# Kernel tuning notes

Hardware: AMD Instinct MI355X
Metric: run time of the kernel (lower is better)

The kernel has to match this reference:

```python
import jax, jax.numpy as jnp
import numpy as np

EMB_DIM = 1024
NUM_HEADS = 16
HEAD_DIM = EMB_DIM // NUM_HEADS


def setup_inputs() -> dict:
    key = jax.random.key(0)
    ks = jax.random.split(key, 10)
    B, Sq, Skv = 4, 4096, 4096
    scale = 1.0 / np.sqrt(EMB_DIM)
    inp = {
        "query": jax.random.normal(ks[0], (B, Sq, EMB_DIM), jnp.float32),
        "key_value": jax.random.normal(ks[1], (B, Skv, EMB_DIM), jnp.float32),
        "Wq": jax.random.normal(ks[2], (EMB_DIM, EMB_DIM), jnp.float32) * scale,
        "bq": jnp.zeros((EMB_DIM,), jnp.float32),
        "Wk": jax.random.normal(ks[3], (EMB_DIM, EMB_DIM), jnp.float32) * scale,
        "bk": jnp.zeros((EMB_DIM,), jnp.float32),
        "Wv": jax.random.normal(ks[4], (EMB_DIM, EMB_DIM), jnp.float32) * scale,
        "bv": jnp.zeros((EMB_DIM,), jnp.float32),
        "Wo": jax.random.normal(ks[5], (EMB_DIM, EMB_DIM), jnp.float32) * scale,
        "bo": jnp.zeros((EMB_DIM,), jnp.float32),
    }
    return inp


def reference(query, key_value, Wq, bq, Wk, bk, Wv, bv, Wo, bo):
    B, Sq, D = query.shape
    Skv = key_value.shape[1]
    H, hd = NUM_HEADS, HEAD_DIM
    # Projections -> [B, S, H, hd]
    Q = (query @ Wq + bq).reshape(B, Sq, H, hd)
    K = (key_value @ Wk + bk).reshape(B, Skv, H, hd)
    V = (key_value @ Wv + bv).reshape(B, Skv, H, hd)
    # elu+1 feature map (strictly positive)
    Q = jax.nn.elu(Q) + 1.0
    K = jax.nn.elu(K) + 1.0
    # KV summarization: [B, H, hd, hd]
    KV = jnp.einsum("bshd,bshe->bhde", K, V)
    K_sum = K.sum(axis=1)  # [B, H, hd]
    # Attention output and normalizer
    out = jnp.einsum("bqhd,bhde->bqhe", Q, KV)          # [B, Sq, H, hd]
    norm = jnp.einsum("bqhd,bhd->bqh", Q, K_sum)         # [B, Sq, H]
    out = out / (norm[..., None] + 1e-6)
    out = out.reshape(B, Sq, D)
    return out @ Wo + bo  # dropout is identity in eval
```

## Files before the change

kernel.cpp:

```cpp
#include <hip/hip_runtime.h>

typedef __bf16 bf16_t;
typedef __bf16 bf16x2 __attribute__((ext_vector_type(2)));
typedef __bf16 bf16x8 __attribute__((ext_vector_type(8)));
typedef float floatx4 __attribute__((ext_vector_type(4)));

#define B_ 4
#define S_ 4096
#define D_ 1024
#define H_ 16
#define HD_ 64
#define M_TOT (B_ * S_)

__device__ __forceinline__ void async_load16(const bf16_t* g, bf16_t* l) {
  __builtin_amdgcn_global_load_lds(
      (const __attribute__((address_space(1))) void*)g,
      (__attribute__((address_space(3))) void*)l,
      16, 0, 0);
}

struct PrepArgs {
  const float* q; const float* kv;
  bf16_t* aq; bf16_t* akv;
  const float* w0; const float* w1; const float* w2; const float* w3;
  bf16_t* t0; bf16_t* t1; bf16_t* t2; bf16_t* t3;
};

__global__ __launch_bounds__(256) void prep_kernel(PrepArgs p) {
  __shared__ float tile[32][33];
  const int bid = blockIdx.x;
  const int t = threadIdx.x;
  if (bid < 16384) {
    const float* in = bid < 8192 ? p.q : p.kv;
    bf16_t* out = bid < 8192 ? p.aq : p.akv;
    int i = ((bid & 8191) * 256 + t) * 8;
    float4 a = *(const float4*)(in + i);
    float4 b = *(const float4*)(in + i + 4);
    bf16x8 o;
    o[0] = (bf16_t)a.x; o[1] = (bf16_t)a.y; o[2] = (bf16_t)a.z; o[3] = (bf16_t)a.w;
    o[4] = (bf16_t)b.x; o[5] = (bf16_t)b.y; o[6] = (bf16_t)b.z; o[7] = (bf16_t)b.w;
    *(bf16x8*)(out + i) = o;
  } else {
    int idx = bid - 16384;
    int z = idx >> 10;
    int rem = idx & 1023;
    const float* W = z == 0 ? p.w0 : z == 1 ? p.w1 : z == 2 ? p.w2 : p.w3;
    bf16_t* Wt = z == 0 ? p.t0 : z == 1 ? p.t1 : z == 2 ? p.t2 : p.t3;
    int n0 = (rem & 31) * 32;
    int k0 = (rem >> 5) * 32;
    int tx = t & 31;
    int ty = t >> 5;
    for (int r = ty; r < 32; r += 8)
      tile[r][tx] = W[(size_t)(k0 + r) * D_ + n0 + tx];
    __syncthreads();
    for (int r = ty; r < 32; r += 8)
      Wt[(size_t)(n0 + r) * D_ + k0 + tx] = (bf16_t)tile[tx][r];
  }
}

__device__ __forceinline__ void gemm256_core(
    const bf16_t* __restrict__ A, const bf16_t* __restrict__ Bt,
    int row0, int col0, bf16_t* As, bf16_t* Bs, floatx4 (&acc)[8][4]) {
  const int tid = threadIdx.x;
  const int w = tid >> 6;
  const int lane = tid & 63;
  const int lr = lane & 15;
  const int lq = lane >> 4;
  const int wm0 = (w >> 2) * 128;
  const int wn0 = (w & 3) * 64;

  const int c0 = w * 64 + lane;
  const int c1 = c0 + 512;
  const int r0 = c0 >> 2, q0 = c0 & 3;
  const int r1 = c1 >> 2, q1 = c1 & 3;
  const size_t offA0 = (size_t)(row0 + r0) * D_ + ((q0 ^ ((r0 >> 1) & 3)) * 8);
  const size_t offA1 = (size_t)(row0 + r1) * D_ + ((q1 ^ ((r1 >> 1) & 3)) * 8);
  const size_t offB0 = (size_t)(col0 + r0) * D_ + ((q0 ^ ((r0 >> 1) & 3)) * 8);
  const size_t offB1 = (size_t)(col0 + r1) * D_ + ((q1 ^ ((r1 >> 1) & 3)) * 8);
  const int ldst0 = w * 512;
  const int ldst1 = 4096 + w * 512;
  const int swz = (lq ^ ((lr >> 1) & 3)) * 8;

#define STAGE_TILE(tt)                                   \
  {                                                      \
    bf16_t* as_ = As + ((tt) & 3) * 8192;                \
    bf16_t* bs_ = Bs + ((tt) & 3) * 8192;                \
    const int ko_ = (tt) * 32;                           \
    async_load16(A + offA0 + ko_, as_ + ldst0);          \
    async_load16(A + offA1 + ko_, as_ + ldst1);          \
    async_load16(Bt + offB0 + ko_, bs_ + ldst0);         \
    async_load16(Bt + offB1 + ko_, bs_ + ldst1);         \
  }

  STAGE_TILE(0)
  STAGE_TILE(1)

  for (int kt = 0; kt < 32; ++kt) {
    if (kt < 30) {
      STAGE_TILE(kt + 2)
      asm volatile("s_waitcnt vmcnt(8)\n\ts_barrier" ::: "memory");
    } else if (kt == 30) {
      asm volatile("s_waitcnt vmcnt(4)\n\ts_barrier" ::: "memory");
    } else {
      asm volatile("s_waitcnt vmcnt(0)\n\ts_barrier" ::: "memory");
    }
    const bf16_t* as = As + (kt & 3) * 8192;
    const bf16_t* bs = Bs + (kt & 3) * 8192;
    bf16x8 af[8], bfr[4];
#pragma unroll
    for (int i = 0; i < 8; ++i)
      af[i] = *(const bf16x8*)&as[(wm0 + i * 16 + lr) * 32 + swz];
#pragma unroll
    for (int j = 0; j < 4; ++j)
      bfr[j] = *(const bf16x8*)&bs[(wn0 + j * 16 + lr) * 32 + swz];
    __builtin_amdgcn_s_setprio(1);
#pragma unroll
    for (int i = 0; i < 8; ++i)
#pragma unroll
      for (int j = 0; j < 4; ++j)
        acc[i][j] = __builtin_amdgcn_mfma_f32_16x16x32_bf16(af[i], bfr[j], acc[i][j], 0, 0, 0);
    __builtin_amdgcn_s_setprio(0);
  }
#undef STAGE_TILE
}

struct ProjArgs {
  const bf16_t* Aq; const bf16_t* Akv;
  const bf16_t* WqT; const bf16_t* WkvT;
  const float* bq; const float* bk; const float* bv;
  bf16_t* Qf; bf16_t* Kf; bf16_t* Vf;
};

__global__ __launch_bounds__(512, 2) void proj256_kernel(ProjArgs p) {
  __shared__ __attribute__((aligned(16))) bf16_t As[4 * 8192];
  __shared__ __attribute__((aligned(16))) bf16_t Bs[4 * 8192];
  const unsigned L = blockIdx.x;
  const unsigned xcd = L & 7;
  const unsigned slot = L >> 3;
  const unsigned mq = slot / 24u;
  const unsigned s24 = slot % 24u;
  const int mt = xcd * 8 + mq * 2 + (s24 & 1);
  const int nt = s24 >> 1;
  const bool isQ = nt < 4;
  const int row0 = mt * 256;
  const int col0 = (isQ ? nt : nt - 4) * 256;
  const bf16_t* A = isQ ? p.Aq : p.Akv;
  const bf16_t* Bt = isQ ? p.WqT : p.WkvT;

  floatx4 acc[8][4];
#pragma unroll
  for (int i = 0; i < 8; ++i)
#pragma unroll
    for (int j = 0; j < 4; ++j) acc[i][j] = (floatx4){0.f, 0.f, 0.f, 0.f};

  gemm256_core(A, Bt, row0, col0, As, Bs, acc);

  const int tid = threadIdx.x;
  const int w = tid >> 6;
  const int lane = tid & 63;
  const int lr = lane & 15;
  const int lq = lane >> 4;
  const int wm0 = (w >> 2) * 128;
  const int wn0 = (w & 3) * 64;

  if (isQ) {
#pragma unroll
    for (int i = 0; i < 8; ++i) {
      int gr = row0 + wm0 + i * 16 + lq * 4;
#pragma unroll
      for (int j = 0; j < 4; ++j) {
        int gc = col0 + wn0 + j * 16 + lr;
        float bsv = p.bq[gc];
#pragma unroll
        for (int r = 0; r < 4; ++r) {
          float v = acc[i][j][r] + bsv;
          v = v > 0.f ? v + 1.f : __expf(v);
          p.Qf[(size_t)(gr + r) * D_ + gc] = (bf16_t)v;
        }
      }
    }
  } else if (nt < 8) {
#pragma unroll
    for (int i = 0; i < 8; ++i) {
      int gr = row0 + wm0 + i * 16 + lq * 4;
#pragma unroll
      for (int j = 0; j < 4; ++j) {
        int gc = col0 + wn0 + j * 16 + lr;
        float bsv = p.bk[gc];
#pragma unroll
        for (int r = 0; r < 4; ++r) {
          float v = acc[i][j][r] + bsv;
          v = v > 0.f ? v + 1.f : __expf(v);
          p.Kf[(size_t)(gr + r) * D_ + gc] = (bf16_t)v;
        }
      }
    }
  } else {
#pragma unroll
    for (int i = 0; i < 8; ++i) {
      int gr = row0 + wm0 + i * 16 + lq * 4;
#pragma unroll
      for (int j = 0; j < 4; ++j) {
        int gc = col0 + wn0 + j * 16 + lr;
        int vc = gc - 1024;
        float bsv = p.bv[vc];
#pragma unroll
        for (int r = 0; r < 4; ++r) {
          float v = acc[i][j][r] + bsv;
          p.Vf[(size_t)(gr + r) * D_ + vc] = (bf16_t)v;
        }
      }
    }
  }
}

__global__ __launch_bounds__(512, 2) void gemm_out256_kernel(
    const bf16_t* __restrict__ A,
    const bf16_t* __restrict__ Bt,
    const float* __restrict__ bias,
    float* __restrict__ outf) {
  __shared__ __attribute__((aligned(16))) bf16_t As[4 * 8192];
  __shared__ __attribute__((aligned(16))) bf16_t Bs[4 * 8192];
  const unsigned L = blockIdx.x;
  const unsigned xcd = L & 7;
  const unsigned slot = L >> 3;
  const unsigned mq = slot >> 3;
  const unsigned s8 = slot & 7;
  const int mt = xcd * 8 + mq * 2 + (s8 & 1);
  const int nt = s8 >> 1;
  const int row0 = mt * 256;
  const int col0 = nt * 256;

  floatx4 acc[8][4];
#pragma unroll
  for (int i = 0; i < 8; ++i)
#pragma unroll
    for (int j = 0; j < 4; ++j) acc[i][j] = (floatx4){0.f, 0.f, 0.f, 0.f};

  gemm256_core(A, Bt, row0, col0, As, Bs, acc);

  const int tid = threadIdx.x;
  const int w = tid >> 6;
  const int lane = tid & 63;
  const int lr = lane & 15;
  const int lq = lane >> 4;
  const int wm0 = (w >> 2) * 128;
  const int wn0 = (w & 3) * 64;

#pragma unroll
  for (int i = 0; i < 8; ++i) {
    int gr = row0 + wm0 + i * 16 + lq * 4;
#pragma unroll
    for (int j = 0; j < 4; ++j) {
      int gc = col0 + wn0 + j * 16 + lr;
      float bsv = bias[gc];
#pragma unroll
      for (int r = 0; r < 4; ++r)
        outf[(size_t)(gr + r) * D_ + gc] = acc[i][j][r] + bsv;
    }
  }
}

#define KVP 68
__global__ __launch_bounds__(256) void kv_mfma_kernel(
    const bf16_t* __restrict__ Kf, const bf16_t* __restrict__ Vf,
    float* __restrict__ KVpart, float* __restrict__ Kspart) {
  __shared__ __attribute__((aligned(16))) bf16_t Kt[64 * KVP];
  __shared__ __attribute__((aligned(16))) bf16_t Vt[64 * KVP];
  const int t = threadIdx.x;
  const int w = t >> 6, lane = t & 63;
  const int lr = lane & 15, lq = lane >> 4;
  const int bh = blockIdx.x, sc = blockIdx.y;
  const int b = bh >> 4, h = bh & 15;
  const size_t base = (size_t)b * S_ * D_ + (size_t)h * HD_;
  const int p = t >> 3;
  const int c0 = (t & 7) * 8;

  floatx4 acc[4], accn[4];
#pragma unroll
  for (int j = 0; j < 4; ++j) {
    acc[j] = (floatx4){0.f, 0.f, 0.f, 0.f};
    accn[j] = (floatx4){0.f, 0.f, 0.f, 0.f};
  }
  bf16x8 ones;
#pragma unroll
  for (int u = 0; u < 8; ++u) ones[u] = (bf16_t)(lr == 0 ? 1.f : 0.f);

  for (int st = 0; st < 8; ++st) {
    int s0 = sc * 512 + st * 64;
    bf16x8 ka = *(const bf16x8*)&Kf[base + (size_t)(s0 + 2 * p) * D_ + c0];
    bf16x8 kb = *(const bf16x8*)&Kf[base + (size_t)(s0 + 2 * p + 1) * D_ + c0];
    bf16x8 va = *(const bf16x8*)&Vf[base + (size_t)(s0 + 2 * p) * D_ + c0];
    bf16x8 vb = *(const bf16x8*)&Vf[base + (size_t)(s0 + 2 * p + 1) * D_ + c0];
    __syncthreads();
#pragma unroll
    for (int u = 0; u < 8; ++u) {
      *(bf16x2*)&Kt[(c0 + u) * KVP + 2 * p] = (bf16x2){ka[u], kb[u]};
      *(bf16x2*)&Vt[(c0 + u) * KVP + 2 * p] = (bf16x2){va[u], vb[u]};
    }
    __syncthreads();
#pragma unroll
    for (int ks = 0; ks < 2; ++ks) {
      bf16x8 af = *(const bf16x8*)&Vt[(w * 16 + lr) * KVP + ks * 32 + lq * 8];
      bf16x8 bf_[4];
#pragma unroll
      for (int j = 0; j < 4; ++j)
        bf_[j] = *(const bf16x8*)&Kt[(j * 16 + lr) * KVP + ks * 32 + lq * 8];
#pragma unroll
      for (int j = 0; j < 4; ++j)
        acc[j] = __builtin_amdgcn_mfma_f32_16x16x32_bf16(af, bf_[j], acc[j], 0, 0, 0);
      if (w == 0) {
#pragma unroll
        for (int j = 0; j < 4; ++j)
          accn[j] = __builtin_amdgcn_mfma_f32_16x16x32_bf16(ones, bf_[j], accn[j], 0, 0, 0);
      }
    }
  }
  float* kvp = KVpart + ((size_t)bh * 8 + sc) * 4096;
#pragma unroll
  for (int j = 0; j < 4; ++j)
#pragma unroll
    for (int r = 0; r < 4; ++r)
      kvp[(w * 16 + lq * 4 + r) * 64 + j * 16 + lr] = acc[j][r];
  if (w == 0 && lq == 0) {
#pragma unroll
    for (int j = 0; j < 4; ++j)
      Kspart[((size_t)bh * 8 + sc) * 64 + j * 16 + lr] = accn[j][0];
  }
}

__global__ __launch_bounds__(256) void kv_reduce_kernel(
    const float* __restrict__ KVpart, const float* __restrict__ Kspart,
    float* __restrict__ KVtg, float* __restrict__ Ksumg) {
  const int bid = blockIdx.x;
  const int t = threadIdx.x;
  if (bid < 256) {
    int idx4 = bid * 256 + t;
    int bh = idx4 >> 10;
    int d4 = idx4 & 1023;
    float4 s = {0.f, 0.f, 0.f, 0.f};
#pragma unroll
    for (int sc = 0; sc < 8; ++sc) {
      float4 v = *(const float4*)&KVpart[((size_t)bh * 8 + sc) * 4096 + d4 * 4];
      s.x += v.x; s.y += v.y; s.z += v.z; s.w += v.w;
    }
    *(float4*)&KVtg[(size_t)bh * 4096 + d4 * 4] = s;
  } else {
    int idx = (bid - 256) * 256 + t;
    int bh = idx >> 4;
    int d4 = idx & 15;
    float4 s = {0.f, 0.f, 0.f, 0.f};
#pragma unroll
    for (int sc = 0; sc < 8; ++sc) {
      float4 v = *(const float4*)&Kspart[((size_t)bh * 8 + sc) * 64 + d4 * 4];
      s.x += v.x; s.y += v.y; s.z += v.z; s.w += v.w;
    }
    *(float4*)&Ksumg[bh * 64 + d4 * 4] = s;
  }
}

__global__ __launch_bounds__(256) void attend_mfma_kernel(
    const bf16_t* __restrict__ Qf, const float* __restrict__ KVtg,
    const float* __restrict__ Ksumg, bf16_t* __restrict__ X) {
  __shared__ __attribute__((aligned(16))) bf16_t As[256 * 64];
  __shared__ __attribute__((aligned(16))) bf16_t Bs[64 * 64];
  const int t = threadIdx.x;
  const int w = t >> 6;
  const int lane = t & 63;
  const int lr = lane & 15;
  const int lq = lane >> 4;
  const int rx = lr & 7;
  const int bh = blockIdx.y;
  const int b = bh >> 4, h = bh & 15;
  const int q0 = blockIdx.x * 256;
  const size_t qbase = ((size_t)b * S_ + q0) * D_ + (size_t)h * HD_;

  {
    const int r8 = lane >> 3;
    const int cs = (((lane & 7) ^ (r8 & 7)) << 3);
#pragma unroll
    for (int it = 0; it < 8; ++it) {
      int r = w * 64 + it * 8 + r8;
      async_load16(&Qf[qbase + (size_t)r * D_ + cs], &As[(w * 64 + it * 8) * 64]);
    }
  }
  {
    const float* src = KVtg + (size_t)bh * 4096;
    int i0 = t * 16;
    float4 f0 = *(const float4*)(src + i0);
    float4 f1 = *(const float4*)(src + i0 + 4);
    float4 f2 = *(const float4*)(src + i0 + 8);
    float4 f3 = *(const float4*)(src + i0 + 12);
    bf16x8 o1, o2;
    o1[0] = (bf16_t)f0.x; o1[1] = (bf16_t)f0.y; o1[2] = (bf16_t)f0.z; o1[3] = (bf16_t)f0.w;
    o1[4] = (bf16_t)f1.x; o1[5] = (bf16_t)f1.y; o1[6] = (bf16_t)f1.z; o1[7] = (bf16_t)f1.w;
    o2[0] = (bf16_t)f2.x; o2[1] = (bf16_t)f2.y; o2[2] = (bf16_t)f2.z; o2[3] = (bf16_t)f2.w;
    o2[4] = (bf16_t)f3.x; o2[5] = (bf16_t)f3.y; o2[6] = (bf16_t)f3.z; o2[7] = (bf16_t)f3.w;
    int r = t >> 2;
    int cc = (t & 3) * 2;
    int rxw = r & 7;
    *(bf16x8*)&Bs[r * 64 + ((cc ^ rxw) << 3)] = o1;
    *(bf16x8*)&Bs[r * 64 + (((cc + 1) ^ rxw) << 3)] = o2;
  }

  bf16x8 bn[2];
#pragma unroll
  for (int ks = 0; ks < 2; ++ks) {
    bf16x8 z;
#pragma unroll
    for (int u = 0; u < 8; ++u) z[u] = (bf16_t)0.f;
    if (lr == 0) {
      const float* kp = &Ksumg[bh * 64 + ks * 32 + lq * 8];
      float4 k1 = *(const float4*)kp;
      float4 k2 = *(const float4*)(kp + 4);
      z[0] = (bf16_t)k1.x; z[1] = (bf16_t)k1.y; z[2] = (bf16_t)k1.z; z[3] = (bf16_t)k1.w;
      z[4] = (bf16_t)k2.x; z[5] = (bf16_t)k2.y; z[6] = (bf16_t)k2.z; z[7] = (bf16_t)k2.w;
    }
    bn[ks] = z;
  }

  floatx4 acc[4][4];
  floatx4 accn[4];
#pragma unroll
  for (int i = 0; i < 4; ++i) {
    accn[i] = (floatx4){0.f, 0.f, 0.f, 0.f};
#pragma unroll
    for (int j = 0; j < 4; ++j) acc[i][j] = (floatx4){0.f, 0.f, 0.f, 0.f};
  }

  __syncthreads();

#pragma unroll
  for (int ks = 0; ks < 2; ++ks) {
    const int go = ((lq + ks * 4) ^ rx) << 3;
    bf16x8 af[4], bfr[4];
#pragma unroll
    for (int i = 0; i < 4; ++i)
      af[i] = *(const bf16x8*)&As[(w * 64 + i * 16 + lr) * 64 + go];
#pragma unroll
    for (int j = 0; j < 4; ++j)
      bfr[j] = *(const bf16x8*)&Bs[(j * 16 + lr) * 64 + go];
#pragma unroll
    for (int i = 0; i < 4; ++i) {
#pragma unroll
      for (int j = 0; j < 4; ++j)
        acc[i][j] = __builtin_amdgcn_mfma_f32_16x16x32_bf16(af[i], bfr[j], acc[i][j], 0, 0, 0);
      accn[i] = __builtin_amdgcn_mfma_f32_16x16x32_bf16(af[i], bn[ks], accn[i], 0, 0, 0);
    }
  }

#pragma unroll
  for (int i = 0; i < 4; ++i) {
    int rowb = q0 + w * 64 + i * 16 + lq * 4;
#pragma unroll
    for (int r = 0; r < 4; ++r) {
      float nr = __shfl(accn[i][r], lane & 48);
      float inv = 1.f / (nr + 1e-6f);
      size_t rb = ((size_t)b * S_ + rowb + r) * D_ + (size_t)h * HD_;
#pragma unroll
      for (int j = 0; j < 4; ++j)
        X[rb + j * 16 + lr] = (bf16_t)(acc[i][j][r] * inv);
    }
  }
}

extern "C" void kernel_launch(void* const* d_in, const int* in_sizes, int n_in,
                              void* d_out, int out_size, void* d_ws, size_t ws_size,
                              hipStream_t stream) {
  const float* query     = (const float*)d_in[0];
  const float* key_value = (const float*)d_in[1];
  const float* Wq = (const float*)d_in[2];
  const float* bq = (const float*)d_in[3];
  const float* Wk = (const float*)d_in[4];
  const float* bk = (const float*)d_in[5];
  const float* Wv = (const float*)d_in[6];
  const float* bv = (const float*)d_in[7];
  const float* Wo = (const float*)d_in[8];
  const float* bo = (const float*)d_in[9];
  float* out = (float*)d_out;

  char* ws = (char*)d_ws;
  const size_t MB = 1024 * 1024;
  bf16_t* Aq   = (bf16_t*)(ws + 0);
  bf16_t* Akv  = (bf16_t*)(ws + 32 * MB);
  float*  KVpart = (float*)(ws + 32 * MB);
  float*  Kspart = (float*)(ws + 40 * MB);
  bf16_t* WqT  = (bf16_t*)(ws + 64 * MB);
  bf16_t* WkT  = (bf16_t*)(ws + 66 * MB);
  bf16_t* WvT  = (bf16_t*)(ws + 68 * MB);
  bf16_t* WoT  = (bf16_t*)(ws + 70 * MB);
  bf16_t* Qf   = (bf16_t*)(ws + 72 * MB);
  bf16_t* Kf   = (bf16_t*)(ws + 104 * MB);
  bf16_t* Vf   = (bf16_t*)(ws + 136 * MB);
  float*  KVtg = (float*)(ws + 168 * MB);
  float*  Ksumg= (float*)(ws + 169 * MB);

  PrepArgs pa = {query, key_value, Aq, Akv, Wq, Wk, Wv, Wo, WqT, WkT, WvT, WoT};
  prep_kernel<<<20480, 256, 0, stream>>>(pa);

  ProjArgs pj = {Aq, Akv, WqT, WkT, bq, bk, bv, Qf, Kf, Vf};
  proj256_kernel<<<768, 512, 0, stream>>>(pj);

  dim3 kvgrid(64, 8);
  kv_mfma_kernel<<<kvgrid, 256, 0, stream>>>(Kf, Vf, KVpart, Kspart);

  kv_reduce_kernel<<<260, 256, 0, stream>>>(KVpart, Kspart, KVtg, Ksumg);

  dim3 agrid(S_ / 256, 64);
  attend_mfma_kernel<<<agrid, 256, 0, stream>>>(Qf, KVtg, Ksumg, Aq );

  gemm_out256_kernel<<<256, 512, 0, stream>>>(Aq, WoT, bo, out);
}
```

Measured before the change: 367.1 us.

## Deepen GEMM prefetch to three tiles and split MFMA loop into two phases

Restructures the 256-tile GEMM main loop to prefetch three k-tiles ahead instead of two, and splits each iteration into two halves that interleave A-tile and B-tile async loads with half of the MFMA work. Fragment register usage drops from 8 A fragments to 4 at a time. The goal is to hide global-load latency better and to spread memory issue across the compute phases. In exchange it adds extra barriers per iteration and more complex waitcnt bookkeeping, which may add sync overhead.

```diff
diff --git a/kernel.cpp b/kernel.cpp
--- a/kernel.cpp
+++ b/kernel.cpp
@@ -69,8 +69,8 @@
   const int wm0 = (w >> 2) * 128;
   const int wn0 = (w & 3) * 64;
 
-  const int c0 = w * 64 + lane;
-  const int c1 = c0 + 512;
+  const int c0 = tid;
+  const int c1 = tid + 512;
   const int r0 = c0 >> 2, q0 = c0 & 3;
   const int r1 = c1 >> 2, q1 = c1 & 3;
   const size_t offA0 = (size_t)(row0 + r0) * D_ + ((q0 ^ ((r0 >> 1) & 3)) * 8);
@@ -81,47 +81,74 @@
   const int ldst1 = 4096 + w * 512;
   const int swz = (lq ^ ((lr >> 1) & 3)) * 8;
 
-#define STAGE_TILE(tt)                                   \
+#define STAGE_A(tt)                                      \
   {                                                      \
     bf16_t* as_ = As + ((tt) & 3) * 8192;                \
-    bf16_t* bs_ = Bs + ((tt) & 3) * 8192;                \
     const int ko_ = (tt) * 32;                           \
     async_load16(A + offA0 + ko_, as_ + ldst0);          \
     async_load16(A + offA1 + ko_, as_ + ldst1);          \
+  }
+#define STAGE_B(tt)                                      \
+  {                                                      \
+    bf16_t* bs_ = Bs + ((tt) & 3) * 8192;                \
+    const int ko_ = (tt) * 32;                           \
     async_load16(Bt + offB0 + ko_, bs_ + ldst0);         \
     async_load16(Bt + offB1 + ko_, bs_ + ldst1);         \
   }
 
-  STAGE_TILE(0)
-  STAGE_TILE(1)
+  STAGE_A(0) STAGE_B(0)
+  STAGE_A(1) STAGE_B(1)
+  STAGE_A(2) STAGE_B(2)
+  asm volatile("s_waitcnt vmcnt(8)\n\ts_barrier" ::: "memory");
 
   for (int kt = 0; kt < 32; ++kt) {
-    if (kt < 30) {
-      STAGE_TILE(kt + 2)
-      asm volatile("s_waitcnt vmcnt(8)\n\ts_barrier" ::: "memory");
-    } else if (kt == 30) {
-      asm volatile("s_waitcnt vmcnt(4)\n\ts_barrier" ::: "memory");
-    } else {
-      asm volatile("s_waitcnt vmcnt(0)\n\ts_barrier" ::: "memory");
-    }
     const bf16_t* as = As + (kt & 3) * 8192;
     const bf16_t* bs = Bs + (kt & 3) * 8192;
-    bf16x8 af[8], bfr[4];
-#pragma unroll
-    for (int i = 0; i < 8; ++i)
+    bf16x8 af[4], bfr[4];
+
+#pragma unroll
+    for (int i = 0; i < 4; ++i)
       af[i] = *(const bf16x8*)&as[(wm0 + i * 16 + lr) * 32 + swz];
 #pragma unroll
     for (int j = 0; j < 4; ++j)
       bfr[j] = *(const bf16x8*)&bs[(wn0 + j * 16 + lr) * 32 + swz];
+    if (kt < 29) STAGE_A(kt + 3)
+    asm volatile("s_barrier" ::: "memory");
+    asm volatile("s_waitcnt lgkmcnt(0)" ::: "memory");
     __builtin_amdgcn_s_setprio(1);
 #pragma unroll
-    for (int i = 0; i < 8; ++i)
+    for (int i = 0; i < 4; ++i)
 #pragma unroll
       for (int j = 0; j < 4; ++j)
         acc[i][j] = __builtin_amdgcn_mfma_f32_16x16x32_bf16(af[i], bfr[j], acc[i][j], 0, 0, 0);
     __builtin_amdgcn_s_setprio(0);
-  }
-#undef STAGE_TILE
+    asm volatile("s_barrier" ::: "memory");
+
+#pragma unroll
+    for (int i = 0; i < 4; ++i)
+      af[i] = *(const bf16x8*)&as[(wm0 + 64 + i * 16 + lr) * 32 + swz];
+    if (kt < 29) {
+      STAGE_B(kt + 3)
+      asm volatile("s_waitcnt vmcnt(8)\n\ts_barrier" ::: "memory");
+    } else if (kt == 29) {
+      asm volatile("s_waitcnt vmcnt(4)\n\ts_barrier" ::: "memory");
+    } else if (kt == 30) {
+      asm volatile("s_waitcnt vmcnt(0)\n\ts_barrier" ::: "memory");
+    } else {
+      asm volatile("s_barrier" ::: "memory");
+    }
+    asm volatile("s_waitcnt lgkmcnt(0)" ::: "memory");
+    __builtin_amdgcn_s_setprio(1);
+#pragma unroll
+    for (int i = 0; i < 4; ++i)
+#pragma unroll
+      for (int j = 0; j < 4; ++j)
+        acc[4 + i][j] = __builtin_amdgcn_mfma_f32_16x16x32_bf16(af[i], bfr[j], acc[4 + i][j], 0, 0, 0);
+    __builtin_amdgcn_s_setprio(0);
+    asm volatile("s_barrier" ::: "memory");
+  }
+#undef STAGE_A
+#undef STAGE_B
 }
 
 struct ProjArgs {
```

Measured after the change: 372.5 us. No clear change (+1.5%).

## Switch GEMMs to 32x32x16 MFMA and emit pre-swizzled bf16 KV summary

Applied to the files above, without the earlier changes.

The shared 256x256 GEMM core now uses 32x32x16 bf16 MFMA tiles with two k-substeps per 32-wide LDS tile instead of 16x16x32 tiles. The epilogues are rewritten for the new accumulator layout. An extra barrier is added at the end of each k-iteration. Separately, the KV reduce kernel now writes the summed KV matrix as bf16 in the swizzled LDS layout, so the attend kernel can async-load it straight into shared memory instead of converting fp32 per block. The MFMA change aims to cut LDS fragment reads per FLOP, though the extra barrier and strided epilogue stores may cost some of that back.

```diff
diff --git a/kernel.cpp b/kernel.cpp
--- a/kernel.cpp
+++ b/kernel.cpp
@@ -4,6 +4,7 @@
 typedef __bf16 bf16x2 __attribute__((ext_vector_type(2)));
 typedef __bf16 bf16x8 __attribute__((ext_vector_type(8)));
 typedef float floatx4 __attribute__((ext_vector_type(4)));
+typedef float floatx16 __attribute__((ext_vector_type(16)));
 
 #define B_ 4
 #define S_ 4096
@@ -60,17 +61,17 @@
 
 __device__ __forceinline__ void gemm256_core(
     const bf16_t* __restrict__ A, const bf16_t* __restrict__ Bt,
-    int row0, int col0, bf16_t* As, bf16_t* Bs, floatx4 (&acc)[8][4]) {
+    int row0, int col0, bf16_t* As, bf16_t* Bs, floatx16 (&acc)[4][2]) {
   const int tid = threadIdx.x;
   const int w = tid >> 6;
   const int lane = tid & 63;
-  const int lr = lane & 15;
-  const int lq = lane >> 4;
+  const int l31 = lane & 31;
+  const int lh = lane >> 5;
   const int wm0 = (w >> 2) * 128;
   const int wn0 = (w & 3) * 64;
 
-  const int c0 = w * 64 + lane;
-  const int c1 = c0 + 512;
+  const int c0 = tid;
+  const int c1 = tid + 512;
   const int r0 = c0 >> 2, q0 = c0 & 3;
   const int r1 = c1 >> 2, q1 = c1 & 3;
   const size_t offA0 = (size_t)(row0 + r0) * D_ + ((q0 ^ ((r0 >> 1) & 3)) * 8);
@@ -79,7 +80,7 @@
   const size_t offB1 = (size_t)(col0 + r1) * D_ + ((q1 ^ ((r1 >> 1) & 3)) * 8);
   const int ldst0 = w * 512;
   const int ldst1 = 4096 + w * 512;
-  const int swz = (lq ^ ((lr >> 1) & 3)) * 8;
+  const int rk = (l31 >> 1) & 3;
 
 #define STAGE_TILE(tt)                                   \
   {                                                      \
@@ -106,20 +107,25 @@
     }
     const bf16_t* as = As + (kt & 3) * 8192;
     const bf16_t* bs = Bs + (kt & 3) * 8192;
-    bf16x8 af[8], bfr[4];
-#pragma unroll
-    for (int i = 0; i < 8; ++i)
-      af[i] = *(const bf16x8*)&as[(wm0 + i * 16 + lr) * 32 + swz];
-#pragma unroll
-    for (int j = 0; j < 4; ++j)
-      bfr[j] = *(const bf16x8*)&bs[(wn0 + j * 16 + lr) * 32 + swz];
-    __builtin_amdgcn_s_setprio(1);
-#pragma unroll
-    for (int i = 0; i < 8; ++i)
-#pragma unroll
-      for (int j = 0; j < 4; ++j)
-        acc[i][j] = __builtin_amdgcn_mfma_f32_16x16x32_bf16(af[i], bfr[j], acc[i][j], 0, 0, 0);
-    __builtin_amdgcn_s_setprio(0);
+#pragma unroll
+    for (int ks = 0; ks < 2; ++ks) {
+      const int pc = ((ks * 2 + lh) ^ rk) << 3;
+      bf16x8 af[4], bfr[2];
+#pragma unroll
+      for (int i = 0; i < 4; ++i)
+        af[i] = *(const bf16x8*)&as[(wm0 + i * 32 + l31) * 32 + pc];
+#pragma unroll
+      for (int j = 0; j < 2; ++j)
+        bfr[j] = *(const bf16x8*)&bs[(wn0 + j * 32 + l31) * 32 + pc];
+      __builtin_amdgcn_s_setprio(1);
+#pragma unroll
+      for (int i = 0; i < 4; ++i)
+#pragma unroll
+        for (int j = 0; j < 2; ++j)
+          acc[i][j] = __builtin_amdgcn_mfma_f32_32x32x16_bf16(af[i], bfr[j], acc[i][j], 0, 0, 0);
+      __builtin_amdgcn_s_setprio(0);
+    }
+    asm volatile("s_barrier" ::: "memory");
   }
 #undef STAGE_TILE
 }
@@ -147,67 +153,64 @@
   const bf16_t* A = isQ ? p.Aq : p.Akv;
   const bf16_t* Bt = isQ ? p.WqT : p.WkvT;
 
-  floatx4 acc[8][4];
-#pragma unroll
-  for (int i = 0; i < 8; ++i)
-#pragma unroll
-    for (int j = 0; j < 4; ++j) acc[i][j] = (floatx4){0.f, 0.f, 0.f, 0.f};
+  floatx16 acc[4][2];
+#pragma unroll
+  for (int i = 0; i < 4; ++i)
+#pragma unroll
+    for (int j = 0; j < 2; ++j)
+#pragma unroll
+      for (int g = 0; g < 16; ++g) acc[i][j][g] = 0.f;
 
   gemm256_core(A, Bt, row0, col0, As, Bs, acc);
 
   const int tid = threadIdx.x;
   const int w = tid >> 6;
   const int lane = tid & 63;
-  const int lr = lane & 15;
-  const int lq = lane >> 4;
+  const int l31 = lane & 31;
+  const int lh = lane >> 5;
   const int wm0 = (w >> 2) * 128;
   const int wn0 = (w & 3) * 64;
 
-  if (isQ) {
-#pragma unroll
-    for (int i = 0; i < 8; ++i) {
-      int gr = row0 + wm0 + i * 16 + lq * 4;
-#pragma unroll
-      for (int j = 0; j < 4; ++j) {
-        int gc = col0 + wn0 + j * 16 + lr;
-        float bsv = p.bq[gc];
-#pragma unroll
-        for (int r = 0; r < 4; ++r) {
-          float v = acc[i][j][r] + bsv;
+#pragma unroll
+  for (int j = 0; j < 2; ++j) {
+    int gc = col0 + wn0 + j * 32 + l31;
+    if (isQ) {
+      float bsv = p.bq[gc];
+#pragma unroll
+      for (int i = 0; i < 4; ++i) {
+        int rb = row0 + wm0 + i * 32 + 4 * lh;
+#pragma unroll
+        for (int g = 0; g < 16; ++g) {
+          int gr = rb + (g & 3) + 8 * (g >> 2);
+          float v = acc[i][j][g] + bsv;
           v = v > 0.f ? v + 1.f : __expf(v);
-          p.Qf[(size_t)(gr + r) * D_ + gc] = (bf16_t)v;
+          p.Qf[(size_t)gr * D_ + gc] = (bf16_t)v;
         }
       }
-    }
-  } else if (nt < 8) {
-#pragma unroll
-    for (int i = 0; i < 8; ++i) {
-      int gr = row0 + wm0 + i * 16 + lq * 4;
-#pragma unroll
-      for (int j = 0; j < 4; ++j) {
-        int gc = col0 + wn0 + j * 16 + lr;
-        float bsv = p.bk[gc];
-#pragma unroll
-        for (int r = 0; r < 4; ++r) {
-          float v = acc[i][j][r] + bsv;
+    } else if (gc < 1024) {
+      float bsv = p.bk[gc];
+#pragma unroll
+      for (int i = 0; i < 4; ++i) {
+        int rb = row0 + wm0 + i * 32 + 4 * lh;
+#pragma unroll
+        for (int g = 0; g < 16; ++g) {
+          int gr = rb + (g & 3) + 8 * (g >> 2);
+          float v = acc[i][j][g] + bsv;
           v = v > 0.f ? v + 1.f : __expf(v);
-          p.Kf[(size_t)(gr + r) * D_ + gc] = (bf16_t)v;
+          p.Kf[(size_t)gr * D_ + gc] = (bf16_t)v;
         }
       }
-    }
-  } else {
-#pragma unroll
-    for (int i = 0; i < 8; ++i) {
-      int gr = row0 + wm0 + i * 16 + lq * 4;
-#pragma unroll
-      for (int j = 0; j < 4; ++j) {
-        int gc = col0 + wn0 + j * 16 + lr;
-        int vc = gc - 1024;
-        float bsv = p.bv[vc];
-#pragma unroll
-        for (int r = 0; r < 4; ++r) {
-          float v = acc[i][j][r] + bsv;
-          p.Vf[(size_t)(gr + r) * D_ + vc] = (bf16_t)v;
+    } else {
+      int vc = gc - 1024;
+      float bsv = p.bv[vc];
+#pragma unroll
+      for (int i = 0; i < 4; ++i) {
+        int rb = row0 + wm0 + i * 32 + 4 * lh;
+#pragma unroll
+        for (int g = 0; g < 16; ++g) {
+          int gr = rb + (g & 3) + 8 * (g >> 2);
+          float v = acc[i][j][g] + bsv;
+          p.Vf[(size_t)gr * D_ + vc] = (bf16_t)v;
         }
       }
     }
@@ -231,32 +234,36 @@
   const int row0 = mt * 256;
   const int col0 = nt * 256;
 
-  floatx4 acc[8][4];
-#pragma unroll
-  for (int i = 0; i < 8; ++i)
-#pragma unroll
-    for (int j = 0; j < 4; ++j) acc[i][j] = (floatx4){0.f, 0.f, 0.f, 0.f};
+  floatx16 acc[4][2];
+#pragma unroll
+  for (int i = 0; i < 4; ++i)
+#pragma unroll
+    for (int j = 0; j < 2; ++j)
+#pragma unroll
+      for (int g = 0; g < 16; ++g) acc[i][j][g] = 0.f;
 
   gemm256_core(A, Bt, row0, col0, As, Bs, acc);
 
   const int tid = threadIdx.x;
   const int w = tid >> 6;
   const int lane = tid & 63;
-  const int lr = lane & 15;
-  const int lq = lane >> 4;
+  const int l31 = lane & 31;
+  const int lh = lane >> 5;
   const int wm0 = (w >> 2) * 128;
   const int wn0 = (w & 3) * 64;
 
 #pragma unroll
-  for (int i = 0; i < 8; ++i) {
-    int gr = row0 + wm0 + i * 16 + lq * 4;
-#pragma unroll
-    for (int j = 0; j < 4; ++j) {
-      int gc = col0 + wn0 + j * 16 + lr;
-      float bsv = bias[gc];
-#pragma unroll
-      for (int r = 0; r < 4; ++r)
-        outf[(size_t)(gr + r) * D_ + gc] = acc[i][j][r] + bsv;
+  for (int j = 0; j < 2; ++j) {
+    int gc = col0 + wn0 + j * 32 + l31;
+    float bsv = bias[gc];
+#pragma unroll
+    for (int i = 0; i < 4; ++i) {
+      int rb = row0 + wm0 + i * 32 + 4 * lh;
+#pragma unroll
+      for (int g = 0; g < 16; ++g) {
+        int gr = rb + (g & 3) + 8 * (g >> 2);
+        outf[(size_t)gr * D_ + gc] = acc[i][j][g] + bsv;
+      }
     }
   }
 }
@@ -331,22 +338,33 @@
 
 __global__ __launch_bounds__(256) void kv_reduce_kernel(
     const float* __restrict__ KVpart, const float* __restrict__ Kspart,
-    float* __restrict__ KVtg, float* __restrict__ Ksumg) {
+    bf16_t* __restrict__ KVb16, float* __restrict__ Ksumg) {
   const int bid = blockIdx.x;
   const int t = threadIdx.x;
-  if (bid < 256) {
-    int idx4 = bid * 256 + t;
-    int bh = idx4 >> 10;
-    int d4 = idx4 & 1023;
-    float4 s = {0.f, 0.f, 0.f, 0.f};
+  if (bid < 128) {
+    int g = bid * 256 + t;
+    int bh = g >> 9;
+    int c = g & 511;
+    int r = c >> 3;
+    int cl = c & 7;
+    int ebase = r * 64 + cl * 8;
+    float s[8];
+#pragma unroll
+    for (int u = 0; u < 8; ++u) s[u] = 0.f;
 #pragma unroll
     for (int sc = 0; sc < 8; ++sc) {
-      float4 v = *(const float4*)&KVpart[((size_t)bh * 8 + sc) * 4096 + d4 * 4];
-      s.x += v.x; s.y += v.y; s.z += v.z; s.w += v.w;
-    }
-    *(float4*)&KVtg[(size_t)bh * 4096 + d4 * 4] = s;
+      const float* src = &KVpart[((size_t)bh * 8 + sc) * 4096 + ebase];
+      float4 v0 = *(const float4*)src;
+      float4 v1 = *(const float4*)(src + 4);
+      s[0] += v0.x; s[1] += v0.y; s[2] += v0.z; s[3] += v0.w;
+      s[4] += v1.x; s[5] += v1.y; s[6] += v1.z; s[7] += v1.w;
+    }
+    bf16x8 o;
+#pragma unroll
+    for (int u = 0; u < 8; ++u) o[u] = (bf16_t)s[u];
+    *(bf16x8*)&KVb16[(size_t)bh * 4096 + r * 64 + ((cl ^ (r & 7)) * 8)] = o;
   } else {
-    int idx = (bid - 256) * 256 + t;
+    int idx = (bid - 128) * 256 + t;
     int bh = idx >> 4;
     int d4 = idx & 15;
     float4 s = {0.f, 0.f, 0.f, 0.f};
@@ -360,7 +378,7 @@
 }
 
 __global__ __launch_bounds__(256) void attend_mfma_kernel(
-    const bf16_t* __restrict__ Qf, const float* __restrict__ KVtg,
+    const bf16_t* __restrict__ Qf, const bf16_t* __restrict__ KVb16,
     const float* __restrict__ Ksumg, bf16_t* __restrict__ X) {
   __shared__ __attribute__((aligned(16))) bf16_t As[256 * 64];
   __shared__ __attribute__((aligned(16))) bf16_t Bs[64 * 64];
@@ -385,22 +403,9 @@
     }
   }
   {
-    const float* src = KVtg + (size_t)bh * 4096;
-    int i0 = t * 16;
-    float4 f0 = *(const float4*)(src + i0);
-    float4 f1 = *(const float4*)(src + i0 + 4);
-    float4 f2 = *(const float4*)(src + i0 + 8);
-    float4 f3 = *(const float4*)(src + i0 + 12);
-    bf16x8 o1, o2;
-    o1[0] = (bf16_t)f0.x; o1[1] = (bf16_t)f0.y; o1[2] = (bf16_t)f0.z; o1[3] = (bf16_t)f0.w;
-    o1[4] = (bf16_t)f1.x; o1[5] = (bf16_t)f1.y; o1[6] = (bf16_t)f1.z; o1[7] = (bf16_t)f1.w;
-    o2[0] = (bf16_t)f2.x; o2[1] = (bf16_t)f2.y; o2[2] = (bf16_t)f2.z; o2[3] = (bf16_t)f2.w;
-    o2[4] = (bf16_t)f3.x; o2[5] = (bf16_t)f3.y; o2[6] = (bf16_t)f3.z; o2[7] = (bf16_t)f3.w;
-    int r = t >> 2;
-    int cc = (t & 3) * 2;
-    int rxw = r & 7;
-    *(bf16x8*)&Bs[r * 64 + ((cc ^ rxw) << 3)] = o1;
-    *(bf16x8*)&Bs[r * 64 + (((cc + 1) ^ rxw) << 3)] = o2;
+    const bf16_t* src = KVb16 + (size_t)bh * 4096;
+    async_load16(&src[(size_t)t * 8], &Bs[w * 512]);
+    async_load16(&src[(size_t)(t + 256) * 8], &Bs[2048 + w * 512]);
   }
 
   bf16x8 bn[2];
@@ -485,6 +490,8 @@
   bf16_t* Akv  = (bf16_t*)(ws + 32 * MB);
   float*  KVpart = (float*)(ws + 32 * MB);
   float*  Kspart = (float*)(ws + 40 * MB);
+  bf16_t* KVb16 = (bf16_t*)(ws + 41 * MB);
+  float*  Ksumg = (float*)(ws + 42 * MB);
   bf16_t* WqT  = (bf16_t*)(ws + 64 * MB);
   bf16_t* WkT  = (bf16_t*)(ws + 66 * MB);
   bf16_t* WvT  = (bf16_t*)(ws + 68 * MB);
@@ -492,8 +499,6 @@
   bf16_t* Qf   = (bf16_t*)(ws + 72 * MB);
   bf16_t* Kf   = (bf16_t*)(ws + 104 * MB);
   bf16_t* Vf   = (bf16_t*)(ws + 136 * MB);
-  float*  KVtg = (float*)(ws + 168 * MB);
-  float*  Ksumg= (float*)(ws + 169 * MB);
 
   PrepArgs pa = {query, key_value, Aq, Akv, Wq, Wk, Wv, Wo, WqT, WkT, WvT, WoT};
   prep_kernel<<<20480, 256, 0, stream>>>(pa);
@@ -504,10 +509,10 @@
   dim3 kvgrid(64, 8);
   kv_mfma_kernel<<<kvgrid, 256, 0, stream>>>(Kf, Vf, KVpart, Kspart);
 
-  kv_reduce_kernel<<<260, 256, 0, stream>>>(KVpart, Kspart, KVtg, Ksumg);
+  kv_reduce_kernel<<<132, 256, 0, stream>>>(KVpart, Kspart, KVb16, Ksumg);
 
   dim3 agrid(S_ / 256, 64);
-  attend_mfma_kernel<<<agrid, 256, 0, stream>>>(Qf, KVtg, Ksumg, Aq );
+  attend_mfma_kernel<<<agrid, 256, 0, stream>>>(Qf, KVb16, Ksumg, Aq );
 
   gemm_out256_kernel<<<256, 512, 0, stream>>>(Aq, WoT, bo, out);
 }
```

Result: slower. 405.9 us (+10.6%).
